# Performance work log

Hardware: AMD Instinct MI355X
Metric: run time of the kernel (lower is better)

Reference implementation:

```python
import math
import jax, jax.numpy as jnp
import numpy as np

HEAD = 16
D_STATE = 12
DT_RANK = 1


def _ln(x, w, b, eps):
    mu = jnp.mean(x, axis=-1, keepdims=True)
    xc = x - mu
    var = jnp.mean(xc * xc, axis=-1, keepdims=True)
    return xc * jax.lax.rsqrt(var + eps) * w + b


def _chan_ln(x, w, b, eps=1e-6):
    # LayerNorm over channel axis of (B, C, H, W)
    return _ln(x.transpose(0, 2, 3, 1), w, b, eps).transpose(0, 3, 1, 2)


def _gconv1x1(x, w):
    # grouped 1x1 conv; x: (B, Cin, H, W), w: (G, Cout_per_g, Cin_per_g)
    B, Cin, H, W = x.shape
    G, Co, Ci = w.shape
    xg = x.reshape(B, G, Ci, H, W)
    y = jnp.einsum('bgihw,goi->bgohw', xg, w)
    return y.reshape(B, G * Co, H, W)


def _dwconv(x, w, b):
    # depthwise 3x3 conv, SAME padding; w: (C, 1, 3, 3)
    y = jax.lax.conv_general_dilated(x, w, (1, 1), 'SAME',
                                     feature_group_count=x.shape[1])
    return y + b[None, :, None, None]


def setup_inputs() -> dict:
    key = jax.random.key(0)
    ks = jax.random.split(key, 16)
    B, C, H, W = 2, 96, 128, 128
    G, E = 24, 192           # groups = C//4, expand_d = 2*C
    c = E // HEAD            # d_inner per head = 12
    R, N = DT_RANK, D_STATE
    f32 = jnp.float32
    inp = {}
    inp['x_rgb'] = jax.random.normal(ks[0], (B, C, H, W), f32)
    inp['x_e'] = jax.random.normal(ks[1], (B, C, H, W), f32)
    inp['in1_w'] = jnp.ones((C,), f32); inp['in1_b'] = jnp.zeros((C,), f32)
    inp['in2_w'] = jnp.ones((C,), f32); inp['in2_b'] = jnp.zeros((C,), f32)
    inp['inproj_rgb_w'] = jax.random.normal(ks[2], (G, E // G, C // G), f32) * 0.2
    inp['inproj_e_w'] = jax.random.normal(ks[3], (G, E // G, C // G), f32) * 0.2
    inp['conv_rgb_w'] = jax.random.normal(ks[4], (E, 1, 3, 3), f32) * 0.2
    inp['conv_rgb_b'] = jnp.zeros((E,), f32)
    inp['conv_e_w'] = jax.random.normal(ks[5], (E, 1, 3, 3), f32) * 0.2
    inp['conv_e_b'] = jnp.zeros((E,), f32)
    inp['xproj_w'] = jax.random.normal(ks[6], (2, R + 2 * N, HEAD), f32) * (HEAD ** -0.5)
    inp['dtproj_w'] = jax.random.uniform(ks[7], (2, HEAD, R), f32, -R ** -0.5, R ** -0.5)
    dt = jnp.exp(jax.random.uniform(ks[8], (2, HEAD), f32)
                 * (math.log(0.1) - math.log(0.001)) + math.log(0.001))
    dt = jnp.clip(dt, 1e-4, None)
    inp['dtproj_b'] = dt + jnp.log(-jnp.expm1(-dt))  # inverse softplus
    inp['A_logs'] = jnp.log(jnp.broadcast_to(jnp.arange(1, N + 1, dtype=f32), (2, HEAD, N)))
    inp['Ds'] = jnp.ones((2, HEAD), f32)
    inp['on1_w'] = jnp.ones((c,), f32); inp['on1_b'] = jnp.zeros((c,), f32)
    inp['on2_w'] = jnp.ones((c,), f32); inp['on2_b'] = jnp.zeros((c,), f32)
    inp['outproj_rgb_w'] = jax.random.normal(ks[9], (G, C // G, E // G), f32) * 0.2
    inp['outproj_e_w'] = jax.random.normal(ks[10], (G, C // G, E // G), f32) * 0.2
    inp['n1_w'] = jnp.ones((C,), f32); inp['n1_b'] = jnp.zeros((C,), f32)
    inp['n2_w'] = jnp.ones((C,), f32); inp['n2_b'] = jnp.zeros((C,), f32)
    Hd = 4 * C
    inp['mlp_rgb_fc1_w'] = jax.random.normal(ks[11], (Hd, C), f32) * 0.1
    inp['mlp_rgb_fc1_b'] = jnp.zeros((Hd,), f32)
    inp['mlp_rgb_fc2_w'] = jax.random.normal(ks[12], (C, Hd), f32) * 0.05
    inp['mlp_rgb_fc2_b'] = jnp.zeros((C,), f32)
    inp['mlp_e_fc1_w'] = jax.random.normal(ks[13], (Hd, C), f32) * 0.1
    inp['mlp_e_fc1_b'] = jnp.zeros((Hd,), f32)
    inp['mlp_e_fc2_w'] = jax.random.normal(ks[14], (C, Hd), f32) * 0.05
    inp['mlp_e_fc2_b'] = jnp.zeros((C,), f32)
    return inp


def reference(x_rgb, x_e, in1_w, in1_b, in2_w, in2_b, inproj_rgb_w, inproj_e_w,
              conv_rgb_w, conv_rgb_b, conv_e_w, conv_e_b, xproj_w, dtproj_w,
              dtproj_b, A_logs, Ds, on1_w, on1_b, on2_w, on2_b,
              outproj_rgb_w, outproj_e_w, n1_w, n1_b, n2_w, n2_b,
              mlp_rgb_fc1_w, mlp_rgb_fc1_b, mlp_rgb_fc2_w, mlp_rgb_fc2_b,
              mlp_e_fc1_w, mlp_e_fc1_b, mlp_e_fc2_w, mlp_e_fc2_b):
    B, C, H, W = x_rgb.shape
    L = H * W
    R, N = DT_RANK, D_STATE
    # input layer norms (eps=1e-6) over channels
    xr = _chan_ln(x_rgb, in1_w, in1_b)
    xe = _chan_ln(x_e, in2_w, in2_b)
    # grouped 1x1 expand + depthwise conv + SiLU
    ur = jax.nn.silu(_dwconv(_gconv1x1(xr, inproj_rgb_w), conv_rgb_w, conv_rgb_b))
    ue = jax.nn.silu(_dwconv(_gconv1x1(xe, inproj_e_w), conv_e_w, conv_e_b))
    c = ur.shape[1] // HEAD  # d_inner per head

    def to_head(x):  # (B, E, H, W) -> (B, L, head, c)
        return x.transpose(0, 2, 3, 1).reshape(B, L, HEAD, c)

    xs = jnp.stack([to_head(ur), to_head(ue)], axis=2)  # (B, L, 2, head, c)
    # input-dependent dt, B, C projections from the per-head feature (dim=head)
    x_dbl = jnp.einsum('blkdc,krd->blkrc', xs, xproj_w)
    dts = x_dbl[..., :R, :]
    Bs = x_dbl[..., R:R + N, :]          # (B, L, 2, N, c)
    Cs = x_dbl[..., R + N:, :]
    dt = jnp.einsum('blkrc,kdr->blkdc', dts, dtproj_w) + dtproj_b[None, None, :, :, None]
    dt = jax.nn.softplus(dt)             # (B, L, 2, head, c)
    A = -jnp.exp(A_logs)                 # (2, head, N)
    Cs_cross = Cs[:, :, ::-1]            # cross-modal readout: swap modalities
    # selective scan over the channel dim c (sequence axis)
    dt_t = jnp.moveaxis(dt, -1, 0)
    u_t = jnp.moveaxis(xs, -1, 0)
    B_t = jnp.moveaxis(Bs, -1, 0)
    C_t = jnp.moveaxis(Cs_cross, -1, 0)
    h0 = jnp.zeros((B, L, 2, HEAD, N), xs.dtype)

    def step(h, inps):
        dt_s, u_s, B_s, C_s = inps
        dA = jnp.exp(dt_s[..., None] * A)                       # (B,L,2,head,N)
        h = dA * h + (dt_s * u_s)[..., None] * B_s[:, :, :, None, :]
        y = jnp.einsum('blkdn,blkn->blkd', h, C_s)
        return h, y

    _, ys = jax.lax.scan(step, h0, (dt_t, u_t, B_t, C_t))
    y = jnp.moveaxis(ys, 0, -1) + xs * Ds[None, None, :, :, None]  # (B,L,2,head,c)
    # per-head LayerNorm over c (eps=1e-5), back to (B, E, H, W)
    y_r = _ln(y[:, :, 0], on1_w, on1_b, 1e-5).reshape(B, H, W, HEAD * c).transpose(0, 3, 1, 2)
    y_e = _ln(y[:, :, 1], on2_w, on2_b, 1e-5).reshape(B, H, W, HEAD * c).transpose(0, 3, 1, 2)
    y_r = _gconv1x1(y_r, outproj_rgb_w) + xr
    y_e = _gconv1x1(y_e, outproj_e_w) + xe

    def mlp(x, nw, nb, w1, b1, w2, b2):
        z = _chan_ln(x, nw, nb)
        z = jnp.einsum('bchw,oc->bohw', z, w1) + b1[None, :, None, None]
        z = jax.nn.gelu(z, approximate=False)
        z = jnp.einsum('bohw,co->bchw', z, w2) + b2[None, :, None, None]
        return x + z

    y_r = mlp(y_r, n1_w, n1_b, mlp_rgb_fc1_w, mlp_rgb_fc1_b, mlp_rgb_fc2_w, mlp_rgb_fc2_b)
    y_e = mlp(y_e, n2_w, n2_b, mlp_e_fc1_w, mlp_e_fc1_b, mlp_e_fc2_w, mlp_e_fc2_b)
    return (y_r, y_e)
```

## Files before the change

kernel.cpp:

```cpp
#include <hip/hip_runtime.h>
#include <math.h>

#define HWn 16384
#define Hn  128
#define Wn  128
#define Bn  2
#define Cn  96
#define En  192
#define Gn  24
#define HEADn 16
#define CCn 12
#define Nn  12
#define HDn 384

#define ZS 68

__global__ __launch_bounds__(256, 4) void k_ln_inproj(
    const float* __restrict__ x0, const float* __restrict__ x1,
    const float* __restrict__ lw0, const float* __restrict__ lb0,
    const float* __restrict__ lw1, const float* __restrict__ lb1,
    const float* __restrict__ pw0, const float* __restrict__ pw1,
    float* __restrict__ xr, float* __restrict__ v)
{
  __shared__ __align__(16) float zn[Cn * ZS];
  __shared__ float red[2 * 16 * 64];
  __shared__ float mus[64], rss[64];

  const int s    = blockIdx.y;
  const int tile = blockIdx.x;
  const int b  = (tile * 64) >> 14;
  const int l0 = (tile * 64) & (HWn - 1);
  const int tid = threadIdx.x;

  const float* x  = s ? x1  : x0;
  const float* lw = s ? lw1 : lw0;
  const float* lb = s ? lb1 : lb0;
  const float* pw = s ? pw1 : pw0;

  const int px4 = (tid & 15) * 4;
  const int cg0 = tid >> 4;

  const float* xp = x + (size_t)b * Cn * HWn + l0;
  float ps0=0.f,ps1=0.f,ps2=0.f,ps3=0.f, pq0=0.f,pq1=0.f,pq2=0.f,pq3=0.f;
#pragma unroll
  for (int i = 0; i < 6; ++i) {
    int ch = cg0 + 16 * i;
    float4 t = *(const float4*)&xp[(size_t)ch * HWn + px4];
    *(float4*)&zn[ch * ZS + px4] = t;
    ps0 += t.x; pq0 += t.x * t.x;
    ps1 += t.y; pq1 += t.y * t.y;
    ps2 += t.z; pq2 += t.z * t.z;
    ps3 += t.w; pq3 += t.w * t.w;
  }
  red[cg0 * 64 + px4 + 0] = ps0; red[1024 + cg0 * 64 + px4 + 0] = pq0;
  red[cg0 * 64 + px4 + 1] = ps1; red[1024 + cg0 * 64 + px4 + 1] = pq1;
  red[cg0 * 64 + px4 + 2] = ps2; red[1024 + cg0 * 64 + px4 + 2] = pq2;
  red[cg0 * 64 + px4 + 3] = ps3; red[1024 + cg0 * 64 + px4 + 3] = pq3;
  __syncthreads();
  if (tid < 64) {
    float sm = 0.f, sq = 0.f;
#pragma unroll
    for (int g = 0; g < 16; ++g) { sm += red[g * 64 + tid]; sq += red[1024 + g * 64 + tid]; }
    float mu = sm * (1.f / Cn);
    float var = sq * (1.f / Cn) - mu * mu;
    mus[tid] = mu; rss[tid] = rsqrtf(var + 1e-6f);
  }
  __syncthreads();

  const float m0 = mus[px4+0], m1 = mus[px4+1], m2 = mus[px4+2], m3 = mus[px4+3];
  const float r0 = rss[px4+0], r1 = rss[px4+1], r2 = rss[px4+2], r3 = rss[px4+3];
  float* xrp = xr + ((size_t)s * Bn + b) * Cn * HWn + l0;
#pragma unroll
  for (int i = 0; i < 6; ++i) {
    int ch = cg0 + 16 * i;
    float4 t = *(const float4*)&zn[ch * ZS + px4];
    float wch = lw[ch], bch = lb[ch];
    t.x = fmaf((t.x - m0) * r0, wch, bch);
    t.y = fmaf((t.y - m1) * r1, wch, bch);
    t.z = fmaf((t.z - m2) * r2, wch, bch);
    t.w = fmaf((t.w - m3) * r3, wch, bch);
    *(float4*)&zn[ch * ZS + px4] = t;
    *(float4*)&xrp[(size_t)ch * HWn + px4] = t;
  }
  __syncthreads();

  const int og  = (tid >> 4) * 12;
  const int pxg = (tid & 15) * 4;
  float* vp = v + ((size_t)s * Bn + b) * En * HWn + l0;
#pragma unroll
  for (int jo = 0; jo < 12; ++jo) {
    int o = og + jo, g = o >> 3;
    float4 wv = *(const float4*)&pw[g * 32 + (o & 7) * 4];
    float4 z0 = *(const float4*)&zn[(g * 4 + 0) * ZS + pxg];
    float4 z1 = *(const float4*)&zn[(g * 4 + 1) * ZS + pxg];
    float4 z2 = *(const float4*)&zn[(g * 4 + 2) * ZS + pxg];
    float4 z3 = *(const float4*)&zn[(g * 4 + 3) * ZS + pxg];
    float4 a;
    a.x = fmaf(z0.x, wv.x, fmaf(z1.x, wv.y, fmaf(z2.x, wv.z, z3.x * wv.w)));
    a.y = fmaf(z0.y, wv.x, fmaf(z1.y, wv.y, fmaf(z2.y, wv.z, z3.y * wv.w)));
    a.z = fmaf(z0.z, wv.x, fmaf(z1.z, wv.y, fmaf(z2.z, wv.z, z3.z * wv.w)));
    a.w = fmaf(z0.w, wv.x, fmaf(z1.w, wv.y, fmaf(z2.w, wv.z, z3.w * wv.w)));
    *(float4*)&vp[(size_t)o * HWn + pxg] = a;
  }
}

__global__ __launch_bounds__(256) void k_dwconv_silu(
    const float* __restrict__ v,
    const float* __restrict__ cw0, const float* __restrict__ cb0,
    const float* __restrict__ cw1, const float* __restrict__ cb1,
    float* __restrict__ u)
{
  const int z = blockIdx.z;
  const int e = blockIdx.y;
  const int p = blockIdx.x * 256 + threadIdx.x;
  const int h = p >> 7, w = p & 127;
  const int s = z >> 1;
  const float* cw  = (s ? cw1 : cw0) + e * 9;
  const float bias = (s ? cb1 : cb0)[e];
  const float* src = v + ((size_t)z * En + e) * HWn;

  float acc = bias;
#pragma unroll
  for (int kh = 0; kh < 3; ++kh) {
    int hh = h + kh - 1;
    if (hh < 0 || hh >= Hn) continue;
#pragma unroll
    for (int kw = 0; kw < 3; ++kw) {
      int ww = w + kw - 1;
      if (ww < 0 || ww >= Wn) continue;
      acc = fmaf(src[hh * Wn + ww], cw[kh * 3 + kw], acc);
    }
  }
  float sig = 1.f / (1.f + expf(-acc));
  u[((size_t)z * En + e) * HWn + p] = acc * sig;
}

#define UPXS 417
#define USS  208
#define UDS  13
#define XPXS 604
#define XSS  300

__global__ __launch_bounds__(512) void k_ssm(
    const float* __restrict__ u_ws, const float* __restrict__ xr_ws,
    float* __restrict__ z_ws,
    const float* __restrict__ xprojw, const float* __restrict__ dtprojw,
    const float* __restrict__ dtprojb, const float* __restrict__ A_logs,
    const float* __restrict__ Ds,
    const float* __restrict__ on1w, const float* __restrict__ on1b,
    const float* __restrict__ on2w, const float* __restrict__ on2b,
    const float* __restrict__ opw0, const float* __restrict__ opw1)
{
  __shared__ __align__(16) float uS[16 * UPXS];
  __shared__ __align__(16) float xdl[16 * XPXS];

  const int tid  = threadIdx.x;
  const int tile = blockIdx.x;
  const int b  = (tile * 16) >> 14;
  const int l0 = (tile * 16) & (HWn - 1);

  const int p2px = tid >> 5, p2s = (tid >> 4) & 1, p2d = tid & 15;
  const float dtw = dtprojw[p2s * HEADn + p2d];
  const float dtb = dtprojb[p2s * HEADn + p2d];
  const float Dv  = Ds[p2s * HEADn + p2d];
  float Ar[Nn];
  {
    const float4* ap = (const float4*)&A_logs[(p2s * HEADn + p2d) * Nn];
    float4 a0 = ap[0], a1 = ap[1], a2 = ap[2];
    Ar[0]=-expf(a0.x); Ar[1]=-expf(a0.y); Ar[2]=-expf(a0.z); Ar[3]=-expf(a0.w);
    Ar[4]=-expf(a1.x); Ar[5]=-expf(a1.y); Ar[6]=-expf(a1.z); Ar[7]=-expf(a1.w);
    Ar[8]=-expf(a2.x); Ar[9]=-expf(a2.y); Ar[10]=-expf(a2.z); Ar[11]=-expf(a2.w);
  }

#pragma unroll
  for (int i = 0; i < 3; ++i) {
    int id = i * 512 + tid;
    int px4 = id & 3, rest = id >> 2;
    int ch = rest % En, s2 = rest / En;
    float4 t = *(const float4*)&u_ws[(((size_t)s2 * Bn + b) * En + ch) * HWn + l0 + px4 * 4];
    int dd = ch / 12, cc = ch % 12;
    int base = s2 * USS + dd * UDS + cc;
    uS[(px4 * 4 + 0) * UPXS + base] = t.x;
    uS[(px4 * 4 + 1) * UPXS + base] = t.y;
    uS[(px4 * 4 + 2) * UPXS + base] = t.z;
    uS[(px4 * 4 + 3) * UPXS + base] = t.w;
  }
  __syncthreads();

#pragma unroll
  for (int j = 0; j < 2; ++j) {
    int id = j * 512 + tid;
    if (id < 800) {
      int px = id & 15, sr = id >> 4;
      int s2 = sr / 25, r = sr % 25;
      const float4* xw4 = (const float4*)&xprojw[(s2 * 25 + r) * HEADn];
      float4 w0 = xw4[0], w1 = xw4[1], w2 = xw4[2], w3 = xw4[3];
      float wv[16];
      wv[0]=w0.x; wv[1]=w0.y; wv[2]=w0.z; wv[3]=w0.w;
      wv[4]=w1.x; wv[5]=w1.y; wv[6]=w1.z; wv[7]=w1.w;
      wv[8]=w2.x; wv[9]=w2.y; wv[10]=w2.z; wv[11]=w2.w;
      wv[12]=w3.x; wv[13]=w3.y; wv[14]=w3.z; wv[15]=w3.w;
      int ub = px * UPXS + s2 * USS;
      float acc[12];
#pragma unroll
      for (int cc = 0; cc < 12; ++cc) acc[cc] = 0.f;
#pragma unroll
      for (int dd = 0; dd < HEADn; ++dd) {
        float w = wv[dd];
        int ua = ub + dd * UDS;
#pragma unroll
        for (int cc = 0; cc < 12; ++cc)
          acc[cc] = fmaf(uS[ua + cc], w, acc[cc]);
      }
      float* xp = &xdl[px * XPXS + s2 * XSS + r * 12];
      *(float4*)&xp[0] = make_float4(acc[0], acc[1], acc[2], acc[3]);
      *(float4*)&xp[4] = make_float4(acc[4], acc[5], acc[6], acc[7]);
      *(float4*)&xp[8] = make_float4(acc[8], acc[9], acc[10], acc[11]);
    }
  }
  __syncthreads();

  {
    const int px = p2px, s = p2s, d = p2d;
    const int ub = px * UPXS + s * USS + d * UDS;
    float uvv[12];
#pragma unroll
    for (int cc = 0; cc < 12; ++cc) uvv[cc] = uS[ub + cc];

    const int xb = px * XPXS;
    float dts[12];
    {
      const float4* dr = (const float4*)&xdl[xb + s * XSS];
      float4 q0 = dr[0], q1 = dr[1], q2 = dr[2];
      dts[0]=q0.x; dts[1]=q0.y; dts[2]=q0.z; dts[3]=q0.w;
      dts[4]=q1.x; dts[5]=q1.y; dts[6]=q1.z; dts[7]=q1.w;
      dts[8]=q2.x; dts[9]=q2.y; dts[10]=q2.z; dts[11]=q2.w;
    }
    float dt_s[12], dtu[12];
#pragma unroll
    for (int cc = 0; cc < 12; ++cc) {
      float pre = fmaf(dts[cc], dtw, dtb);
      float v = (pre > 20.f) ? pre : log1pf(expf(pre));
      dt_s[cc] = v;
      dtu[cc] = v * uvv[cc];
    }

    float y[12];
#pragma unroll
    for (int cc = 0; cc < 12; ++cc) y[cc] = 0.f;

#pragma unroll
    for (int n = 0; n < Nn; ++n) {
      const float4* Br = (const float4*)&xdl[xb + s * XSS + (1 + n) * 12];
      const float4* Cr = (const float4*)&xdl[xb + (1 - s) * XSS + (13 + n) * 12];
      float4 b0 = Br[0], b1 = Br[1], b2 = Br[2];
      float4 c0 = Cr[0], c1 = Cr[1], c2 = Cr[2];
      float Bv[12], Cv[12];
      Bv[0]=b0.x; Bv[1]=b0.y; Bv[2]=b0.z; Bv[3]=b0.w;
      Bv[4]=b1.x; Bv[5]=b1.y; Bv[6]=b1.z; Bv[7]=b1.w;
      Bv[8]=b2.x; Bv[9]=b2.y; Bv[10]=b2.z; Bv[11]=b2.w;
      Cv[0]=c0.x; Cv[1]=c0.y; Cv[2]=c0.z; Cv[3]=c0.w;
      Cv[4]=c1.x; Cv[5]=c1.y; Cv[6]=c1.z; Cv[7]=c1.w;
      Cv[8]=c2.x; Cv[9]=c2.y; Cv[10]=c2.z; Cv[11]=c2.w;
      float h = 0.f;
      float An = Ar[n];
#pragma unroll
      for (int cc = 0; cc < 12; ++cc) {
        float dA = expf(dt_s[cc] * An);
        h = fmaf(dA, h, dtu[cc] * Bv[cc]);
        y[cc] = fmaf(h, Cv[cc], y[cc]);
      }
    }

#pragma unroll
    for (int cc = 0; cc < 12; ++cc) y[cc] = fmaf(uvv[cc], Dv, y[cc]);

    float mu = 0.f;
#pragma unroll
    for (int cc = 0; cc < 12; ++cc) mu += y[cc];
    mu *= (1.f / CCn);
    float var = 0.f;
#pragma unroll
    for (int cc = 0; cc < 12; ++cc) { float t = y[cc] - mu; var = fmaf(t, t, var); }
    var *= (1.f / CCn);
    float rs = rsqrtf(var + 1e-5f);
    const float* ow = s ? on2w : on1w;
    const float* ob = s ? on2b : on1b;
#pragma unroll
    for (int cc = 0; cc < 12; ++cc)
      uS[ub + cc] = fmaf((y[cc] - mu) * rs, ow[cc], ob[cc]);
  }
  __syncthreads();

#pragma unroll
  for (int i = 0; i < 2; ++i) {
    int id = i * 512 + tid;
    if (id < 768) {
      int px4 = id & 3, ch = (id >> 2) % Cn, ss = id / 384;
      int g = ch >> 2, co = ch & 3;
      const float* ow2 = (ss ? opw1 : opw0) + g * 32 + co * 8;
      float a0 = 0.f, a1 = 0.f, a2 = 0.f, a3 = 0.f;
#pragma unroll
      for (int ci = 0; ci < 8; ++ci) {
        int e = g * 8 + ci;
        int dd = e / 12, cc = e % 12;
        int base = ss * USS + dd * UDS + cc;
        float w = ow2[ci];
        a0 = fmaf(uS[(px4 * 4 + 0) * UPXS + base], w, a0);
        a1 = fmaf(uS[(px4 * 4 + 1) * UPXS + base], w, a1);
        a2 = fmaf(uS[(px4 * 4 + 2) * UPXS + base], w, a2);
        a3 = fmaf(uS[(px4 * 4 + 3) * UPXS + base], w, a3);
      }
      size_t go = (((size_t)ss * Bn + b) * Cn + ch) * HWn + l0 + px4 * 4;
      float4 xrv = *(const float4*)&xr_ws[go];
      *(float4*)&z_ws[go] =
          make_float4(a0 + xrv.x, a1 + xrv.y, a2 + xrv.z, a3 + xrv.w);
    }
  }
}

__global__ void k_transpose_w(
    const float* __restrict__ w1r, const float* __restrict__ w1e,
    const float* __restrict__ w2r, const float* __restrict__ w2e,
    float* __restrict__ w1t, float* __restrict__ w2t)
{
  int idx = blockIdx.x * 256 + threadIdx.x;
  int which = idx / 36864;
  int r = idx % 36864;
  if (which < 2) {
    int c = r / HDn, o = r % HDn;
    const float* src = which ? w1e : w1r;
    w1t[which * 36864 + r] = src[o * Cn + c];
  } else {
    int o = r / Cn, c = r % Cn;
    const float* src = (which == 3) ? w2e : w2r;
    w2t[(which - 2) * 36864 + r] = src[c * HDn + o];
  }
}

#define HSS 34

__global__ __launch_bounds__(256, 4) void k_mlp(
    const float* __restrict__ z_all,
    const float* __restrict__ n1w, const float* __restrict__ n1b,
    const float* __restrict__ n2w, const float* __restrict__ n2b,
    const float* __restrict__ w1t_all, const float* __restrict__ b1r,
    const float* __restrict__ b1e,
    const float* __restrict__ w2t_all, const float* __restrict__ b2r,
    const float* __restrict__ b2e,
    float* __restrict__ out_all)
{
  __shared__ float zn[Cn * 32];
  __shared__ float hS[192 * HSS];
  __shared__ float red[2 * 8 * 32];
  __shared__ float mus[32], rss[32];

  const int s    = blockIdx.y;
  const int tile = blockIdx.x;
  const int b    = (tile * 32) >> 14;
  const int l0   = (tile * 32) & (HWn - 1);
  const int tid  = threadIdx.x;

  const float* z   = z_all + ((size_t)s * Bn + b) * Cn * HWn + l0;
  float*       out = (float*)out_all + ((size_t)s * Bn + b) * Cn * HWn + l0;
  const float* nw  = s ? n2w : n1w;
  const float* nb  = s ? n2b : n1b;
  const float* w1t = w1t_all + s * 36864;
  const float* b1  = s ? b1e : b1r;
  const float* w2t = w2t_all + s * 36864;
  const float* b2  = s ? b2e : b2r;

  {
    const int px = tid & 31, part = tid >> 5;
    float psum = 0.f, pss = 0.f;
#pragma unroll
    for (int i = 0; i < 12; ++i) {
      int c = part + 8 * i;
      float v = z[(size_t)c * HWn + px];
      zn[c * 32 + px] = v; psum += v; pss += v * v;
    }
    red[part * 32 + px] = psum;
    red[256 + part * 32 + px] = pss;
    __syncthreads();
    if (tid < 32) {
      float sm = 0.f, sq = 0.f;
#pragma unroll
      for (int p = 0; p < 8; ++p) { sm += red[p * 32 + tid]; sq += red[256 + p * 32 + tid]; }
      float mu = sm * (1.f / Cn);
      float var = sq * (1.f / Cn) - mu * mu;
      mus[tid] = mu; rss[tid] = rsqrtf(var + 1e-6f);
    }
    __syncthreads();
    float mu = mus[px], rs = rss[px];
#pragma unroll
    for (int i = 0; i < 12; ++i) {
      int c = part + 8 * i;
      float v = zn[c * 32 + px];
      zn[c * 32 + px] = fmaf((v - mu) * rs, nw[c], nb[c]);
    }
    __syncthreads();
  }

  const int pg   = (tid & 7) << 2;
  const int og   = (tid >> 3) * 6;
  const int p2px = (tid & 15) * 2;
  const int cg   = (tid >> 4) * 6;

  float a2[6][2];
#pragma unroll
  for (int k = 0; k < 6; ++k) { a2[k][0] = 0.f; a2[k][1] = 0.f; }

#pragma unroll
  for (int hf = 0; hf < 2; ++hf) {
    float acc[6][4];
#pragma unroll
    for (int j = 0; j < 6; ++j)
#pragma unroll
      for (int i = 0; i < 4; ++i) acc[j][i] = 0.f;

    const float* w1base = w1t + hf * 192 + og;
    for (int c = 0; c < Cn; ++c) {
      float4 xv = *(const float4*)&zn[c * 32 + pg];
      const float* wr = w1base + c * HDn;
      float2 wa = *(const float2*)&wr[0];
      float2 wb = *(const float2*)&wr[2];
      float2 wc = *(const float2*)&wr[4];
      float w[6] = {wa.x, wa.y, wb.x, wb.y, wc.x, wc.y};
#pragma unroll
      for (int j = 0; j < 6; ++j) {
        acc[j][0] = fmaf(xv.x, w[j], acc[j][0]);
        acc[j][1] = fmaf(xv.y, w[j], acc[j][1]);
        acc[j][2] = fmaf(xv.z, w[j], acc[j][2]);
        acc[j][3] = fmaf(xv.w, w[j], acc[j][3]);
      }
    }
#pragma unroll
    for (int j = 0; j < 6; ++j) {
      float bo = b1[hf * 192 + og + j];
      float g0 = acc[j][0] + bo, g1 = acc[j][1] + bo;
      float g2 = acc[j][2] + bo, g3 = acc[j][3] + bo;
      g0 = 0.5f * g0 * (1.f + erff(g0 * 0.70710678118654752f));
      g1 = 0.5f * g1 * (1.f + erff(g1 * 0.70710678118654752f));
      g2 = 0.5f * g2 * (1.f + erff(g2 * 0.70710678118654752f));
      g3 = 0.5f * g3 * (1.f + erff(g3 * 0.70710678118654752f));
      float* hr = &hS[(og + j) * HSS + pg];
      *(float2*)&hr[0] = make_float2(g0, g1);
      *(float2*)&hr[2] = make_float2(g2, g3);
    }
    __syncthreads();

    const float* w2base = w2t + (hf * 192) * Cn + cg;
    for (int o = 0; o < 192; ++o) {
      float2 hv = *(const float2*)&hS[o * HSS + p2px];
      const float* wr = w2base + o * Cn;
      float2 wa = *(const float2*)&wr[0];
      float2 wb = *(const float2*)&wr[2];
      float2 wc = *(const float2*)&wr[4];
      a2[0][0] = fmaf(hv.x, wa.x, a2[0][0]); a2[0][1] = fmaf(hv.y, wa.x, a2[0][1]);
      a2[1][0] = fmaf(hv.x, wa.y, a2[1][0]); a2[1][1] = fmaf(hv.y, wa.y, a2[1][1]);
      a2[2][0] = fmaf(hv.x, wb.x, a2[2][0]); a2[2][1] = fmaf(hv.y, wb.x, a2[2][1]);
      a2[3][0] = fmaf(hv.x, wb.y, a2[3][0]); a2[3][1] = fmaf(hv.y, wb.y, a2[3][1]);
      a2[4][0] = fmaf(hv.x, wc.x, a2[4][0]); a2[4][1] = fmaf(hv.y, wc.x, a2[4][1]);
      a2[5][0] = fmaf(hv.x, wc.y, a2[5][0]); a2[5][1] = fmaf(hv.y, wc.y, a2[5][1]);
    }
    __syncthreads();
  }

#pragma unroll
  for (int k = 0; k < 6; ++k) {
    int c = cg + k;
    float bk = b2[c];
    size_t off = (size_t)c * HWn + p2px;
    float2 zv = *(const float2*)&z[off];
    *(float2*)&out[off] = make_float2(a2[k][0] + bk + zv.x, a2[k][1] + bk + zv.y);
  }
}

extern "C" void kernel_launch(void* const* d_in, const int* in_sizes, int n_in,
                              void* d_out, int out_size, void* d_ws, size_t ws_size,
                              hipStream_t stream)
{
  const float* x_rgb = (const float*)d_in[0];
  const float* x_e   = (const float*)d_in[1];
  const float* in1_w = (const float*)d_in[2];
  const float* in1_b = (const float*)d_in[3];
  const float* in2_w = (const float*)d_in[4];
  const float* in2_b = (const float*)d_in[5];
  const float* ipw0  = (const float*)d_in[6];
  const float* ipw1  = (const float*)d_in[7];
  const float* cw0   = (const float*)d_in[8];
  const float* cb0   = (const float*)d_in[9];
  const float* cw1   = (const float*)d_in[10];
  const float* cb1   = (const float*)d_in[11];
  const float* xprojw  = (const float*)d_in[12];
  const float* dtprojw = (const float*)d_in[13];
  const float* dtprojb = (const float*)d_in[14];
  const float* A_logs  = (const float*)d_in[15];
  const float* Ds      = (const float*)d_in[16];
  const float* on1w  = (const float*)d_in[17];
  const float* on1b  = (const float*)d_in[18];
  const float* on2w  = (const float*)d_in[19];
  const float* on2b  = (const float*)d_in[20];
  const float* opw0  = (const float*)d_in[21];
  const float* opw1  = (const float*)d_in[22];
  const float* n1w   = (const float*)d_in[23];
  const float* n1b   = (const float*)d_in[24];
  const float* n2w   = (const float*)d_in[25];
  const float* n2b   = (const float*)d_in[26];
  const float* w1r   = (const float*)d_in[27];
  const float* b1r   = (const float*)d_in[28];
  const float* w2r   = (const float*)d_in[29];
  const float* b2r   = (const float*)d_in[30];
  const float* w1e   = (const float*)d_in[31];
  const float* b1e   = (const float*)d_in[32];
  const float* w2e   = (const float*)d_in[33];
  const float* b2e   = (const float*)d_in[34];

  float* ws  = (float*)d_ws;
  float* xr  = ws;
  float* vz  = ws + (size_t)6291456;
  float* ut  = ws + (size_t)18874368;
  float* w1t = ut;
  float* w2t = ut + 73728;

  dim3 b256(256);

  k_ln_inproj<<<dim3(512, 2), b256, 0, stream>>>(
      x_rgb, x_e, in1_w, in1_b, in2_w, in2_b, ipw0, ipw1, xr, vz);

  k_dwconv_silu<<<dim3(64, En, 4), b256, 0, stream>>>(
      vz, cw0, cb0, cw1, cb1, ut);

  k_ssm<<<dim3(2048), dim3(512), 0, stream>>>(
      ut, xr, vz, xprojw, dtprojw, dtprojb, A_logs, Ds,
      on1w, on1b, on2w, on2b, opw0, opw1);

  k_transpose_w<<<dim3(576), b256, 0, stream>>>(w1r, w1e, w2r, w2e, w1t, w2t);

  k_mlp<<<dim3(1024, 2), b256, 0, stream>>>(
      vz, n1w, n1b, n2w, n2b, w1t, b1r, b1e, w2t, b2r, b2e, (float*)d_out);
}
```

Before: 669.3 us.

## Restructure MLP kernel: single-pass fc1 with full hidden tile, direct fc2 weights

The MLP kernel now computes all 384 hidden channels in one pass, giving each thread 12 outputs by 4 pixels and using float4 weight loads. The full hidden activation tile goes into shared memory, so the second half-pass and its extra barriers disappear. fc2 reads the original (untransposed) weight rows with float4 loads over the hidden dimension, and the w2 transpose work is removed from the prep kernel. Launch bounds drop to 2 blocks per SM, and the larger shared footprint and register use may reduce occupancy. Output stores become scalar and strided per pixel.

```diff
diff --git a/kernel.cpp b/kernel.cpp
--- a/kernel.cpp
+++ b/kernel.cpp
@@ -319,39 +319,32 @@
   }
 }
 
-__global__ void k_transpose_w(
+__global__ void k_transpose_w1(
     const float* __restrict__ w1r, const float* __restrict__ w1e,
-    const float* __restrict__ w2r, const float* __restrict__ w2e,
-    float* __restrict__ w1t, float* __restrict__ w2t)
+    float* __restrict__ w1t)
 {
   int idx = blockIdx.x * 256 + threadIdx.x;
-  int which = idx / 36864;
-  int r = idx % 36864;
-  if (which < 2) {
+  if (idx < 2 * 36864) {
+    int which = idx / 36864;
+    int r = idx % 36864;
     int c = r / HDn, o = r % HDn;
     const float* src = which ? w1e : w1r;
-    w1t[which * 36864 + r] = src[o * Cn + c];
-  } else {
-    int o = r / Cn, c = r % Cn;
-    const float* src = (which == 3) ? w2e : w2r;
-    w2t[(which - 2) * 36864 + r] = src[c * HDn + o];
+    w1t[idx] = src[o * Cn + c];
   }
 }
 
-#define HSS 34
-
-__global__ __launch_bounds__(256, 4) void k_mlp(
+__global__ __launch_bounds__(256, 2) void k_mlp(
     const float* __restrict__ z_all,
     const float* __restrict__ n1w, const float* __restrict__ n1b,
     const float* __restrict__ n2w, const float* __restrict__ n2b,
     const float* __restrict__ w1t_all, const float* __restrict__ b1r,
     const float* __restrict__ b1e,
-    const float* __restrict__ w2t_all, const float* __restrict__ b2r,
-    const float* __restrict__ b2e,
+    const float* __restrict__ w2r_, const float* __restrict__ w2e_,
+    const float* __restrict__ b2r, const float* __restrict__ b2e,
     float* __restrict__ out_all)
 {
-  __shared__ float zn[Cn * 32];
-  __shared__ float hS[192 * HSS];
+  __shared__ __align__(16) float zn[Cn * 32];
+  __shared__ __align__(16) float hS[HDn * 32];
   __shared__ float red[2 * 8 * 32];
   __shared__ float mus[32], rss[32];
 
@@ -367,7 +360,7 @@
   const float* nb  = s ? n2b : n1b;
   const float* w1t = w1t_all + s * 36864;
   const float* b1  = s ? b1e : b1r;
-  const float* w2t = w2t_all + s * 36864;
+  const float* w2  = s ? w2e_ : w2r_;
   const float* b2  = s ? b2e : b2r;
 
   {
@@ -401,33 +394,26 @@
     __syncthreads();
   }
 
-  const int pg   = (tid & 7) << 2;
-  const int og   = (tid >> 3) * 6;
-  const int p2px = (tid & 15) * 2;
-  const int cg   = (tid >> 4) * 6;
-
-  float a2[6][2];
-#pragma unroll
-  for (int k = 0; k < 6; ++k) { a2[k][0] = 0.f; a2[k][1] = 0.f; }
-
-#pragma unroll
-  for (int hf = 0; hf < 2; ++hf) {
-    float acc[6][4];
-#pragma unroll
-    for (int j = 0; j < 6; ++j)
+  const int pg = (tid & 7) << 2;
+
+  {
+    const int og = (tid >> 3) * 12;
+    float acc[12][4];
+#pragma unroll
+    for (int j = 0; j < 12; ++j)
 #pragma unroll
       for (int i = 0; i < 4; ++i) acc[j][i] = 0.f;
 
-    const float* w1base = w1t + hf * 192 + og;
+#pragma unroll 2
     for (int c = 0; c < Cn; ++c) {
       float4 xv = *(const float4*)&zn[c * 32 + pg];
-      const float* wr = w1base + c * HDn;
-      float2 wa = *(const float2*)&wr[0];
-      float2 wb = *(const float2*)&wr[2];
-      float2 wc = *(const float2*)&wr[4];
-      float w[6] = {wa.x, wa.y, wb.x, wb.y, wc.x, wc.y};
-#pragma unroll
-      for (int j = 0; j < 6; ++j) {
+      const float4* wr = (const float4*)&w1t[c * HDn + og];
+      float4 wq0 = wr[0], wq1 = wr[1], wq2 = wr[2];
+      float w[12] = {wq0.x, wq0.y, wq0.z, wq0.w,
+                     wq1.x, wq1.y, wq1.z, wq1.w,
+                     wq2.x, wq2.y, wq2.z, wq2.w};
+#pragma unroll
+      for (int j = 0; j < 12; ++j) {
         acc[j][0] = fmaf(xv.x, w[j], acc[j][0]);
         acc[j][1] = fmaf(xv.y, w[j], acc[j][1]);
         acc[j][2] = fmaf(xv.z, w[j], acc[j][2]);
@@ -435,44 +421,61 @@
       }
     }
 #pragma unroll
-    for (int j = 0; j < 6; ++j) {
-      float bo = b1[hf * 192 + og + j];
+    for (int j = 0; j < 12; ++j) {
+      float bo = b1[og + j];
       float g0 = acc[j][0] + bo, g1 = acc[j][1] + bo;
       float g2 = acc[j][2] + bo, g3 = acc[j][3] + bo;
       g0 = 0.5f * g0 * (1.f + erff(g0 * 0.70710678118654752f));
       g1 = 0.5f * g1 * (1.f + erff(g1 * 0.70710678118654752f));
       g2 = 0.5f * g2 * (1.f + erff(g2 * 0.70710678118654752f));
       g3 = 0.5f * g3 * (1.f + erff(g3 * 0.70710678118654752f));
-      float* hr = &hS[(og + j) * HSS + pg];
-      *(float2*)&hr[0] = make_float2(g0, g1);
-      *(float2*)&hr[2] = make_float2(g2, g3);
-    }
-    __syncthreads();
-
-    const float* w2base = w2t + (hf * 192) * Cn + cg;
-    for (int o = 0; o < 192; ++o) {
-      float2 hv = *(const float2*)&hS[o * HSS + p2px];
-      const float* wr = w2base + o * Cn;
-      float2 wa = *(const float2*)&wr[0];
-      float2 wb = *(const float2*)&wr[2];
-      float2 wc = *(const float2*)&wr[4];
-      a2[0][0] = fmaf(hv.x, wa.x, a2[0][0]); a2[0][1] = fmaf(hv.y, wa.x, a2[0][1]);
-      a2[1][0] = fmaf(hv.x, wa.y, a2[1][0]); a2[1][1] = fmaf(hv.y, wa.y, a2[1][1]);
-      a2[2][0] = fmaf(hv.x, wb.x, a2[2][0]); a2[2][1] = fmaf(hv.y, wb.x, a2[2][1]);
-      a2[3][0] = fmaf(hv.x, wb.y, a2[3][0]); a2[3][1] = fmaf(hv.y, wb.y, a2[3][1]);
-      a2[4][0] = fmaf(hv.x, wc.x, a2[4][0]); a2[4][1] = fmaf(hv.y, wc.x, a2[4][1]);
-      a2[5][0] = fmaf(hv.x, wc.y, a2[5][0]); a2[5][1] = fmaf(hv.y, wc.y, a2[5][1]);
-    }
-    __syncthreads();
-  }
-
-#pragma unroll
-  for (int k = 0; k < 6; ++k) {
-    int c = cg + k;
-    float bk = b2[c];
-    size_t off = (size_t)c * HWn + p2px;
-    float2 zv = *(const float2*)&z[off];
-    *(float2*)&out[off] = make_float2(a2[k][0] + bk + zv.x, a2[k][1] + bk + zv.y);
+      *(float4*)&hS[(og + j) * 32 + pg] = make_float4(g0, g1, g2, g3);
+    }
+  }
+  __syncthreads();
+
+  {
+    const int cg = (tid >> 3) * 3;
+    float a0[4], a1[4], a2[4];
+#pragma unroll
+    for (int i = 0; i < 4; ++i) { a0[i] = 0.f; a1[i] = 0.f; a2[i] = 0.f; }
+
+    const float* w2s0 = w2 + (size_t)(cg + 0) * HDn;
+    const float* w2s1 = w2 + (size_t)(cg + 1) * HDn;
+    const float* w2s2 = w2 + (size_t)(cg + 2) * HDn;
+
+    for (int o4 = 0; o4 < HDn; o4 += 4) {
+      float4 h0 = *(const float4*)&hS[(o4 + 0) * 32 + pg];
+      float4 h1 = *(const float4*)&hS[(o4 + 1) * 32 + pg];
+      float4 h2 = *(const float4*)&hS[(o4 + 2) * 32 + pg];
+      float4 h3 = *(const float4*)&hS[(o4 + 3) * 32 + pg];
+      float4 wA = *(const float4*)&w2s0[o4];
+      float4 wB = *(const float4*)&w2s1[o4];
+      float4 wC = *(const float4*)&w2s2[o4];
+      a0[0] = fmaf(h3.x, wA.w, fmaf(h2.x, wA.z, fmaf(h1.x, wA.y, fmaf(h0.x, wA.x, a0[0]))));
+      a0[1] = fmaf(h3.y, wA.w, fmaf(h2.y, wA.z, fmaf(h1.y, wA.y, fmaf(h0.y, wA.x, a0[1]))));
+      a0[2] = fmaf(h3.z, wA.w, fmaf(h2.z, wA.z, fmaf(h1.z, wA.y, fmaf(h0.z, wA.x, a0[2]))));
+      a0[3] = fmaf(h3.w, wA.w, fmaf(h2.w, wA.z, fmaf(h1.w, wA.y, fmaf(h0.w, wA.x, a0[3]))));
+      a1[0] = fmaf(h3.x, wB.w, fmaf(h2.x, wB.z, fmaf(h1.x, wB.y, fmaf(h0.x, wB.x, a1[0]))));
+      a1[1] = fmaf(h3.y, wB.w, fmaf(h2.y, wB.z, fmaf(h1.y, wB.y, fmaf(h0.y, wB.x, a1[1]))));
+      a1[2] = fmaf(h3.z, wB.w, fmaf(h2.z, wB.z, fmaf(h1.z, wB.y, fmaf(h0.z, wB.x, a1[2]))));
+      a1[3] = fmaf(h3.w, wB.w, fmaf(h2.w, wB.z, fmaf(h1.w, wB.y, fmaf(h0.w, wB.x, a1[3]))));
+      a2[0] = fmaf(h3.x, wC.w, fmaf(h2.x, wC.z, fmaf(h1.x, wC.y, fmaf(h0.x, wC.x, a2[0]))));
+      a2[1] = fmaf(h3.y, wC.w, fmaf(h2.y, wC.z, fmaf(h1.y, wC.y, fmaf(h0.y, wC.x, a2[1]))));
+      a2[2] = fmaf(h3.z, wC.w, fmaf(h2.z, wC.z, fmaf(h1.z, wC.y, fmaf(h0.z, wC.x, a2[2]))));
+      a2[3] = fmaf(h3.w, wC.w, fmaf(h2.w, wC.z, fmaf(h1.w, wC.y, fmaf(h0.w, wC.x, a2[3]))));
+    }
+#pragma unroll
+    for (int k = 0; k < 3; ++k) {
+      int c = cg + k;
+      float bk = b2[c];
+      const float* ak = (k == 0) ? a0 : (k == 1) ? a1 : a2;
+#pragma unroll
+      for (int i = 0; i < 4; ++i) {
+        size_t off = (size_t)c * HWn + pg + i;
+        out[off] = ak[i] + bk + z[off];
+      }
+    }
   }
 }
 
@@ -521,7 +524,6 @@
   float* vz  = ws + (size_t)6291456;
   float* ut  = ws + (size_t)18874368;
   float* w1t = ut;
-  float* w2t = ut + 73728;
 
   dim3 b256(256);
 
@@ -535,8 +537,8 @@
       ut, xr, vz, xprojw, dtprojw, dtprojb, A_logs, Ds,
       on1w, on1b, on2w, on2b, opw0, opw1);
 
-  k_transpose_w<<<dim3(576), b256, 0, stream>>>(w1r, w1e, w2r, w2e, w1t, w2t);
+  k_transpose_w1<<<dim3(288), b256, 0, stream>>>(w1r, w1e, w1t);
 
   k_mlp<<<dim3(1024, 2), b256, 0, stream>>>(
-      vz, n1w, n1b, n2w, n2b, w1t, b1r, b1e, w2t, b2r, b2e, (float*)d_out);
+      vz, n1w, n1b, n2w, n2b, w1t, b1r, b1e, w2r, w2e, b2r, b2e, (float*)d_out);
 }
```

Measured after the change: 566.0 us. 15.4% less time.
